# Performance work log

Hardware: AMD Instinct MI355X
Metric: run time of the kernel (lower is better)

The kernel has to match this reference:

```python
import jax, jax.numpy as jnp
import numpy as np

D = 2048
NH = 16
DH = D // NH          # 128
DC = D // 4           # 512  (KV latent)
DCQ = D // 2          # 1024 (Q latent)
B = 1
L = 2048
MAX_LEN = 4096


def precompute_rope(dh, max_len):
    inv_freq = 1.0 / (10000.0 ** (jnp.arange(0, dh, 2, dtype=jnp.float32) / dh))
    t = jnp.arange(max_len, dtype=jnp.float32)
    freqs = jnp.outer(t, inv_freq)                 # [max_len, dh/2]
    emb = jnp.concatenate([freqs, freqs], axis=-1) # [max_len, dh]
    return jnp.cos(emb), jnp.sin(emb)


def apply_rope(t, cos, sin):
    # t: [B, H, L, dh]; cos/sin: [L, dh]
    x1, x2 = jnp.split(t, 2, axis=-1)
    rot = jnp.concatenate([-x2, x1], axis=-1)
    return t * cos + rot * sin


def setup_inputs() -> dict:
    key = jax.random.key(0)
    ks = jax.random.split(key, 9)
    s = 0.02
    return {
        "x": jax.random.normal(ks[0], (B, L, D), dtype=jnp.float32),
        "W_DKV": jax.random.normal(ks[1], (D, DC), dtype=jnp.float32) * s,
        "W_UK": jax.random.normal(ks[2], (DC, NH * DH), dtype=jnp.float32) * s,
        "W_UV": jax.random.normal(ks[3], (DC, NH * DH), dtype=jnp.float32) * s,
        "W_DQ": jax.random.normal(ks[4], (D, DCQ), dtype=jnp.float32) * s,
        "W_UQ": jax.random.normal(ks[5], (DCQ, 2 * NH * DH), dtype=jnp.float32) * s,
        "W_lam": jax.random.normal(ks[6], (D, NH), dtype=jnp.float32) * s,
        "b_lam": jnp.zeros((NH,), dtype=jnp.float32),
        "W_out": jax.random.normal(ks[7], (D, D), dtype=jnp.float32) * s,
    }


def reference(x, W_DKV, W_UK, W_UV, W_DQ, W_UQ, W_lam, b_lam, W_out):
    Bx, Lx, Dx = x.shape
    cos, sin = precompute_rope(DH, MAX_LEN)
    cos, sin = cos[:Lx], sin[:Lx]

    # MLA KV compression: single K/V shared by the paired query heads
    c_kv = x @ W_DKV                                            # [B, L, dc]
    k = (c_kv @ W_UK).reshape(Bx, Lx, NH, DH).transpose(0, 2, 1, 3)   # [B, nh, L, dh]
    v = (c_kv @ W_UV).reshape(Bx, Lx, NH, DH).transpose(0, 2, 1, 3)   # [B, nh, L, dh]

    # Low-rank Q, doubled heads for differential attention
    c_q = x @ W_DQ                                              # [B, L, dcq]
    q = (c_q @ W_UQ).reshape(Bx, Lx, 2 * NH, DH).transpose(0, 2, 1, 3)  # [B, 2nh, L, dh]

    q = apply_rope(q, cos, sin)
    k = apply_rope(k, cos, sin)

    # Group paired heads (2i, 2i+1) share k/v head i -> avoid repeat_interleave
    qp = q.reshape(Bx, NH, 2, Lx, DH)                           # [B, nh, 2, L, dh]
    scale = 1.0 / jnp.sqrt(jnp.asarray(DH, dtype=x.dtype))
    scores = jnp.einsum('bhpqd,bhkd->bhpqk', qp, k) * scale     # [B, nh, 2, L, L]
    causal = jnp.tril(jnp.ones((Lx, Lx), dtype=bool))
    scores = jnp.where(causal, scores, jnp.asarray(-jnp.inf, dtype=scores.dtype))
    probs = jax.nn.softmax(scores, axis=-1)
    attn = jnp.einsum('bhpqk,bhkd->bhpqd', probs, v)            # [B, nh, 2, L, dh]
    attn1, attn2 = attn[:, :, 0], attn[:, :, 1]                 # [B, nh, L, dh]

    # Token-specific sigmoid lambda per head
    lam = jax.nn.sigmoid(x @ W_lam + b_lam)                     # [B, L, nh]
    lam = lam.transpose(0, 2, 1)[..., None]                     # [B, nh, L, 1]

    out = (attn1 - lam * attn2).transpose(0, 2, 1, 3).reshape(Bx, Lx, Dx)
    return out @ W_out
```

## Files before the change

kernel.cpp:

```cpp
#include <hip/hip_runtime.h>
#include <cstdint>
#include <cstddef>

typedef __bf16 bf16x8 __attribute__((ext_vector_type(8)));
typedef __bf16 bf16x4 __attribute__((ext_vector_type(4)));
typedef float f32x4 __attribute__((ext_vector_type(4)));


template <int N> __device__ __forceinline__ void waitcnt_vm() {
  if constexpr (N == 3)      asm volatile("s_waitcnt vmcnt(3)" ::: "memory");
  else if constexpr (N == 4) asm volatile("s_waitcnt vmcnt(4)" ::: "memory");
  else if constexpr (N == 6) asm volatile("s_waitcnt vmcnt(6)" ::: "memory");
  else if constexpr (N == 8) asm volatile("s_waitcnt vmcnt(8)" ::: "memory");
  else                       asm volatile("s_waitcnt vmcnt(0)" ::: "memory");
}

template <int BM, int NKS>
__device__ __forceinline__ void gemm_core(const __bf16* __restrict__ A,
                                          const __bf16* __restrict__ Bt,
                                          int K, int bm, int bn,
                                          __bf16* As, __bf16* Bs,
                                          f32x4 (*acc)[4]) {
  const int tid = threadIdx.x;
  const int w = tid >> 6;
  const int lane = tid & 63;
  const int quad = lane >> 4;
  const int l16 = lane & 15;
  constexpr int WM = (BM == 128) ? 64 : 32;
  constexpr int MI = WM / 16;
  constexpr int NL = NKS * (BM / 64 + 2);
  const int wm = (w & 1) * WM;
  const int wn = (w >> 1) * 64;
  const int srow = lane >> 2;
  const int sseg = (lane & 3) * 8;

  auto stage = [&](int k0, int buf) {
#pragma unroll
    for (int ks = 0; ks < NKS; ++ks) {
#pragma unroll
      for (int g = 0; g < BM / 64; ++g) {
        const int grp = w + g * 4;
        const __bf16* ga = A + (size_t)(bm + grp * 16 + srow) * K + k0 + ks * 32 + sseg;
        __builtin_amdgcn_global_load_lds(
            (const __attribute__((address_space(1))) void*)ga,
            (__attribute__((address_space(3))) void*)&As[(buf * NKS + ks) * (BM * 32) + grp * 512],
            16, 0, 0);
      }
#pragma unroll
      for (int g = 0; g < 2; ++g) {
        const int grp = w + g * 4;
        const __bf16* gb = Bt + (size_t)(bn + grp * 16 + srow) * K + k0 + ks * 32 + sseg;
        __builtin_amdgcn_global_load_lds(
            (const __attribute__((address_space(1))) void*)gb,
            (__attribute__((address_space(3))) void*)&Bs[(buf * NKS + ks) * 4096 + grp * 512],
            16, 0, 0);
      }
    }
  };

#pragma unroll
  for (int i = 0; i < MI; ++i)
#pragma unroll
    for (int j = 0; j < 4; ++j) acc[i][j] = (f32x4){0.f, 0.f, 0.f, 0.f};

  asm volatile("s_waitcnt vmcnt(0)" ::: "memory");
  stage(0, 0);

  const int NIT = K / (32 * NKS);
  for (int it = 0; it < NIT; ++it) {
    const int cur = it & 1;
    if (it + 1 < NIT) {
      stage((it + 1) * 32 * NKS, cur ^ 1);
      waitcnt_vm<NL>();
    } else {
      waitcnt_vm<0>();
    }
    __builtin_amdgcn_s_barrier();
    asm volatile("" ::: "memory");
    const __bf16* Ab = &As[cur * NKS * (BM * 32)];
    const __bf16* Bb = &Bs[cur * NKS * 4096];
#pragma unroll
    for (int ks = 0; ks < NKS; ++ks) {
      bf16x8 af[MI], bfr[4];
#pragma unroll
      for (int i = 0; i < MI; ++i)
        af[i] = *(const bf16x8*)&Ab[ks * (BM * 32) + (wm + i * 16 + l16) * 32 + quad * 8];
#pragma unroll
      for (int j = 0; j < 4; ++j)
        bfr[j] = *(const bf16x8*)&Bb[ks * 4096 + (wn + j * 16 + l16) * 32 + quad * 8];
#pragma unroll
      for (int i = 0; i < MI; ++i)
#pragma unroll
        for (int j = 0; j < 4; ++j)
          acc[i][j] = __builtin_amdgcn_mfma_f32_16x16x32_bf16(af[i], bfr[j],
                                                              acc[i][j], 0, 0, 0);
    }
    asm volatile("s_waitcnt lgkmcnt(0)" ::: "memory");
    __builtin_amdgcn_s_barrier();
    asm volatile("" ::: "memory");
  }
}

template <int BM, int NKS, bool BF16OUT>
__device__ __forceinline__ void gemm_body(const __bf16* __restrict__ A,
                                          const __bf16* __restrict__ Bt,
                                          void* __restrict__ Cv,
                                          int N, int K, int bm, int bn,
                                          __bf16* As, __bf16* Bs) {
  constexpr int MI = (BM == 128) ? 4 : 2;
  constexpr int WM = (BM == 128) ? 64 : 32;
  f32x4 acc[MI][4];
  gemm_core<BM, NKS>(A, Bt, K, bm, bn, As, Bs, acc);
  const int tid = threadIdx.x;
  const int w = tid >> 6, lane = tid & 63, quad = lane >> 4, l16 = lane & 15;
  const int wm = (w & 1) * WM, wn = (w >> 1) * 64;
#pragma unroll
  for (int i = 0; i < MI; ++i)
#pragma unroll
    for (int j = 0; j < 4; ++j)
#pragma unroll
      for (int r = 0; r < 4; ++r) {
        const int row = bm + wm + i * 16 + quad * 4 + r;
        const int col = bn + wn + j * 16 + l16;
        if constexpr (BF16OUT)
          ((__bf16*)Cv)[(size_t)row * N + col] = (__bf16)acc[i][j][r];
        else
          ((float*)Cv)[(size_t)row * N + col] = acc[i][j][r];
      }
}

template <int BM, int NKS, bool BF16OUT>
__global__ __launch_bounds__(256) void gemm_mfma(const __bf16* __restrict__ A,
                                                 const __bf16* __restrict__ Bt,
                                                 void* __restrict__ Cv,
                                                 int M, int N, int K) {
  __shared__ __bf16 As[2 * BM * 32 * NKS];
  __shared__ __bf16 Bs[2 * 128 * 32 * NKS];
  gemm_body<BM, NKS, BF16OUT>(A, Bt, Cv, N, K, blockIdx.y * BM, blockIdx.x * 128, As, Bs);
}

__global__ __launch_bounds__(256) void down_lam(
    const __bf16* __restrict__ x_bf, const __bf16* __restrict__ WtDKV,
    const __bf16* __restrict__ WtDQ, __bf16* __restrict__ c_kv,
    __bf16* __restrict__ c_q, const __bf16* __restrict__ WlT,
    const float* __restrict__ b_lam, float* __restrict__ lam) {
  __shared__ __bf16 As[2 * 64 * 32 * 2];
  __shared__ __bf16 Bs[2 * 128 * 32 * 2];
  const int bx = blockIdx.x;
  const int tid = threadIdx.x;
  if (bx == 12) {
    const int w = tid >> 6, lane = tid & 63, quad = lane >> 4, l16 = lane & 15;
    const int m0 = (blockIdx.y * 4 + w) * 16;
    const __bf16* xrow = x_bf + (size_t)(m0 + l16) * 2048 + quad * 8;
    const __bf16* wrow = WlT + (size_t)l16 * 2048 + quad * 8;
    f32x4 acc[4];
#pragma unroll
    for (int u = 0; u < 4; ++u) acc[u] = (f32x4){0.f, 0.f, 0.f, 0.f};
    for (int k0 = 0; k0 < 2048; k0 += 128) {
#pragma unroll
      for (int u = 0; u < 4; ++u) {
        bf16x8 a = *(const bf16x8*)&xrow[k0 + u * 32];
        bf16x8 b = *(const bf16x8*)&wrow[k0 + u * 32];
        acc[u] = __builtin_amdgcn_mfma_f32_16x16x32_bf16(a, b, acc[u], 0, 0, 0);
      }
    }
    const float bl = b_lam[l16];
#pragma unroll
    for (int r = 0; r < 4; ++r) {
      const float v = acc[0][r] + acc[1][r] + acc[2][r] + acc[3][r] + bl;
      lam[(size_t)(m0 + quad * 4 + r) * 16 + l16] = 1.0f / (1.0f + __expf(-v));
    }
    return;
  }
  if (bx < 4)
    gemm_body<64, 2, true>(x_bf, WtDKV, (void*)c_kv, 512, 2048,
                           blockIdx.y * 64, bx * 128, As, Bs);
  else
    gemm_body<64, 2, true>(x_bf, WtDQ, (void*)c_q, 1024, 2048,
                           blockIdx.y * 64, (bx - 4) * 128, As, Bs);
}

__global__ __launch_bounds__(256) void up_fused3(
    const __bf16* __restrict__ c_kv, const __bf16* __restrict__ WtUK,
    const __bf16* __restrict__ WtUV, const __bf16* __restrict__ c_q,
    const __bf16* __restrict__ WtUQ, __bf16* __restrict__ k_bf,
    __bf16* __restrict__ v_t, __bf16* __restrict__ q_bf,
    const float* __restrict__ cosT, const float* __restrict__ sinT) {
  __shared__ __align__(16) char usm[32768];
  __bf16* As = (__bf16*)usm;
  __bf16* Bs = (__bf16*)(usm + 16384);
  const int bx = blockIdx.x;
  const int bm = blockIdx.y * 128;
  const int tid = threadIdx.x;
  const int w = tid >> 6, lane = tid & 63, quad = lane >> 4, l16 = lane & 15;
  const int wm = (w & 1) * 64, wn = (w >> 1) * 64;
  f32x4 acc[4][4];
  if (bx < 16) {
    const int bn = bx * 128;
    gemm_core<128, 1>(c_kv, WtUK, 512, bm, bn, As, Bs, acc);
    __bf16 (*Kt)[128] = (__bf16(*)[128])usm;
#pragma unroll
    for (int i = 0; i < 4; ++i)
#pragma unroll
      for (int j = 0; j < 4; ++j)
#pragma unroll
        for (int r = 0; r < 4; ++r)
          Kt[wm + i * 16 + quad * 4 + r][wn + j * 16 + l16] = (__bf16)acc[i][j][r];
    __syncthreads();
#pragma unroll
    for (int j = 0; j < 4; ++j) {
      const int d = wn + j * 16 + l16;
      const float sgn = (d < 64) ? -1.f : 1.f;
#pragma unroll
      for (int i = 0; i < 4; ++i)
#pragma unroll
        for (int r = 0; r < 4; ++r) {
          const int lr = wm + i * 16 + quad * 4 + r;
          const int l = bm + lr;
          const float v = (float)Kt[lr][d];
          const float pr = (float)Kt[lr][d ^ 64];
          const float ov = v * cosT[l * 128 + d] + sgn * pr * sinT[l * 128 + d];
          k_bf[(size_t)l * 2048 + bn + d] = (__bf16)ov;
        }
    }
  } else if (bx < 32) {
    const int bn = (bx - 16) * 128;
    gemm_core<128, 1>(c_kv, WtUV, 512, bm, bn, As, Bs, acc);
#pragma unroll
    for (int i = 0; i < 4; ++i)
#pragma unroll
      for (int j = 0; j < 4; ++j) {
        const int d = bn + wn + j * 16 + l16;
        const int l = bm + wm + i * 16 + quad * 4;
        bf16x4 pk = {(__bf16)acc[i][j][0], (__bf16)acc[i][j][1],
                     (__bf16)acc[i][j][2], (__bf16)acc[i][j][3]};
        *(bf16x4*)&v_t[(size_t)d * 2048 + l] = pk;
      }
  } else {
    const int bn = (bx - 32) * 128;
    gemm_core<128, 1>(c_q, WtUQ, 1024, bm, bn, As, Bs, acc);
#pragma unroll
    for (int i = 0; i < 4; ++i)
#pragma unroll
      for (int j = 0; j < 4; ++j)
#pragma unroll
        for (int r = 0; r < 4; ++r) {
          const int row = bm + wm + i * 16 + quad * 4 + r;
          const int col = bn + wn + j * 16 + l16;
          q_bf[(size_t)row * 4096 + col] = (__bf16)acc[i][j][r];
        }
  }
}

__global__ __launch_bounds__(256) void prep_all(
    const float* __restrict__ W_DKV, const float* __restrict__ W_DQ,
    const float* __restrict__ W_UK,  const float* __restrict__ W_UV,
    const float* __restrict__ W_UQ,  const float* __restrict__ W_out,
    const float* __restrict__ x,     const float* __restrict__ W_lam,
    __bf16* __restrict__ tDKV, __bf16* __restrict__ tDQ,
    __bf16* __restrict__ tUK,  __bf16* __restrict__ tUV,
    __bf16* __restrict__ tUQ,  __bf16* __restrict__ tOut,
    __bf16* __restrict__ x_bf, __bf16* __restrict__ WlT,
    float* __restrict__ cosT, float* __restrict__ sinT) {
  __shared__ float T[32][36];
  int t = blockIdx.x;
  const int tid = threadIdx.x;
  if (t < 13312) {
    const float* src; __bf16* dst; int K, N, kx, ny;
    if (t < 1024)      {            src = W_DKV; dst = tDKV; K = 2048; N = 512;  kx = t & 63; ny = t >> 6; }
    else if (t < 3072) { t -= 1024; src = W_DQ;  dst = tDQ;  K = 2048; N = 1024; kx = t & 63; ny = t >> 6; }
    else if (t < 4096) { t -= 3072; src = W_UK;  dst = tUK;  K = 512;  N = 2048; kx = t & 15; ny = t >> 4; }
    else if (t < 5120) { t -= 4096; src = W_UV;  dst = tUV;  K = 512;  N = 2048; kx = t & 15; ny = t >> 4; }
    else if (t < 9216) { t -= 5120; src = W_UQ;  dst = tUQ;  K = 1024; N = 4096; kx = t & 31; ny = t >> 5; }
    else               { t -= 9216; src = W_out; dst = tOut; K = 2048; N = 2048; kx = t & 63; ny = t >> 6; }
    const int k0 = kx * 32;
    const int n0 = ny * 32;
    const int r = tid >> 3;
    const int c = (tid & 7) * 4;
    *(float4*)&T[r][c] = *(const float4*)&src[(size_t)(k0 + r) * N + n0 + c];
    __syncthreads();
    bf16x4 o = {(__bf16)T[c + 0][r], (__bf16)T[c + 1][r],
                (__bf16)T[c + 2][r], (__bf16)T[c + 3][r]};
    *(bf16x4*)&dst[(size_t)(n0 + r) * K + k0 + c] = o;
    return;
  }
  t -= 13312;
  if (t < 4096) {
    const int i = t * 256 + tid;
    float4 v = *(const float4*)&x[(size_t)i * 4];
    bf16x4 o = {(__bf16)v.x, (__bf16)v.y, (__bf16)v.z, (__bf16)v.w};
    *(bf16x4*)&x_bf[(size_t)i * 4] = o;
    return;
  }
  t -= 4096;
  if (t < 1024) {
    const int l = t * 2 + (tid >> 7);
    const int d = tid & 127;
    const int j = d & 63;
    const float inv = exp2f(-(float)j * 0.2076205059304601f);
    const float ang = (float)l * inv;
    cosT[l * 128 + d] = cosf(ang);
    sinT[l * 128 + d] = sinf(ang);
    return;
  }
  t -= 1024;
  {
    const int i = t * 256 + tid;
    const int k = i >> 4, n = i & 15;
    WlT[(size_t)n * 2048 + k] = (__bf16)W_lam[i];
  }
}

__global__ __launch_bounds__(512, 2) void attn_kernel3(
    const __bf16* __restrict__ Qb, const __bf16* __restrict__ Kb,
    const __bf16* __restrict__ Vt, const float* __restrict__ cosT,
    const float* __restrict__ sinT, const float* __restrict__ lam,
    __bf16* __restrict__ y) {
  __shared__ __align__(16) char smem[81920];
  float (*Ex)[132] = (float(*)[132])smem;

  const int bx = blockIdx.x;
  const int qt = 31 - (bx >> 4);
  const int hk = bx & 15;
  const int q0 = qt * 64;
  const int tid = threadIdx.x;
  const int w = tid >> 6, lane = tid & 63, quad = lane >> 4, l16 = lane & 15;
  const int wrow = (w & 3) * 16;
  const int qoff = (2 * hk + (w >> 2)) * 128;
  const int kvoff = hk * 128;
  const float qscale = 0.08838834764831845f;
  char* Pw = smem + 65536 + w * 2048;

  bf16x8 aq[4];
  {
    const int l = q0 + wrow + l16;
    const size_t qbase = (size_t)l * 4096 + qoff + quad * 8;
    bf16x8 raw[4];
#pragma unroll
    for (int ks = 0; ks < 4; ++ks)
      raw[ks] = *(const bf16x8*)&Qb[qbase + ks * 32];
#pragma unroll
    for (int ks = 0; ks < 4; ++ks) {
      const float* cp = &cosT[l * 128 + ks * 32 + quad * 8];
      const float* sp = &sinT[l * 128 + ks * 32 + quad * 8];
#pragma unroll
      for (int j = 0; j < 8; ++j) {
        const float cv = cp[j];
        const float sv = sp[j];
        const float rot = (ks < 2) ? -(float)raw[ks + 2][j] : (float)raw[ks - 2][j];
        aq[ks][j] = (__bf16)(((float)raw[ks][j] * cv + rot * sv) * qscale);
      }
    }
  }

  auto stage = [&](int kt_, char* buf) {
    const int k0_ = kt_ * 64;
    __bf16* Ksb = (__bf16*)buf;
    __bf16* Vsb = (__bf16*)(buf + 16384);
#pragma unroll
    for (int d = 0; d < 2; ++d) {
      const int r0 = w * 8 + d * 4;
      const int row = r0 + (lane >> 4);
      const int ck = (lane & 15) ^ (row & 15);
      const __bf16* ga = Kb + (size_t)(k0_ + row) * 2048 + kvoff + ck * 8;
      __builtin_amdgcn_global_load_lds(
          (const __attribute__((address_space(1))) void*)ga,
          (__attribute__((address_space(3))) void*)&Ksb[r0 * 128], 16, 0, 0);
      const int r0v = w * 16 + d * 8;
      const int rowv = r0v + (lane >> 3);
      const int cv = (lane & 7) ^ (rowv & 7);
      const __bf16* gv = Vt + (size_t)(kvoff + rowv) * 2048 + k0_ + cv * 8;
      __builtin_amdgcn_global_load_lds(
          (const __attribute__((address_space(1))) void*)gv,
          (__attribute__((address_space(3))) void*)&Vsb[r0v * 64], 16, 0, 0);
    }
  };

  f32x4 o[8];
#pragma unroll
  for (int i = 0; i < 8; ++i) o[i] = (f32x4){0.f, 0.f, 0.f, 0.f};
  float m = -1e30f, lsum = 0.f;

  asm volatile("s_waitcnt vmcnt(0)" ::: "memory");
  stage(0, smem);

  for (int kt = 0; kt <= qt; ++kt) {
    const int cur = kt & 1;
    __bf16* Ks = (__bf16*)(smem + cur * 32768);
    __bf16* Vs = (__bf16*)(smem + cur * 32768 + 16384);
    const int k0 = kt * 64;
    if (kt < qt) {
      stage(kt + 1, smem + (cur ^ 1) * 32768);
      asm volatile("s_waitcnt vmcnt(4)" ::: "memory");
    } else {
      asm volatile("s_waitcnt vmcnt(0)" ::: "memory");
    }
    __builtin_amdgcn_s_barrier();
    asm volatile("" ::: "memory");
    f32x4 st[4];
#pragma unroll
    for (int t = 0; t < 4; ++t) st[t] = (f32x4){0.f, 0.f, 0.f, 0.f};
    __builtin_amdgcn_s_setprio(1);
#pragma unroll
    for (int ks = 0; ks < 4; ++ks) {
#pragma unroll
      for (int t = 0; t < 4; ++t) {
        bf16x8 ak = *(bf16x8*)&Ks[(t * 16 + l16) * 128 + (((ks * 4 + quad) ^ l16) << 3)];
        st[t] = __builtin_amdgcn_mfma_f32_16x16x32_bf16(ak, aq[ks], st[t], 0, 0, 0);
      }
    }
    __builtin_amdgcn_s_setprio(0);
    {
      const int q = q0 + wrow + l16;
      float rm = -1e30f;
      if (kt != qt) {
#pragma unroll
        for (int t = 0; t < 4; ++t)
#pragma unroll
          for (int r = 0; r < 4; ++r) rm = fmaxf(rm, st[t][r]);
      } else {
#pragma unroll
        for (int t = 0; t < 4; ++t)
#pragma unroll
          for (int r = 0; r < 4; ++r) {
            const int key = k0 + t * 16 + quad * 4 + r;
            if (key > q) st[t][r] = -1e30f;
            rm = fmaxf(rm, st[t][r]);
          }
      }
      rm = fmaxf(rm, __shfl_xor(rm, 16, 64));
      rm = fmaxf(rm, __shfl_xor(rm, 32, 64));
      const float mn = fmaxf(m, rm);
      float rs = 0.f;
#pragma unroll
      for (int t = 0; t < 4; ++t)
#pragma unroll
        for (int r = 0; r < 4; ++r) {
          st[t][r] = __expf(st[t][r] - mn);
          rs += st[t][r];
        }
      rs += __shfl_xor(rs, 16, 64);
      rs += __shfl_xor(rs, 32, 64);
      if (__any(rm > m)) {
        const float alpha = __expf(m - mn);
        lsum = lsum * alpha + rs;
        m = mn;
#pragma unroll
        for (int r = 0; r < 4; ++r) {
          const float ar = __shfl(alpha, quad * 4 + r, 64);
#pragma unroll
          for (int nt = 0; nt < 8; ++nt) o[nt][r] *= ar;
        }
      } else {
        lsum += rs;
      }
      const int prow = l16;
#pragma unroll
      for (int t = 0; t < 4; ++t) {
        bf16x4 pk = {(__bf16)st[t][0], (__bf16)st[t][1],
                     (__bf16)st[t][2], (__bf16)st[t][3]};
        const int wch = (t * 2 + (quad >> 1)) ^ (prow & 7);
        *(bf16x4*)(Pw + prow * 128 + wch * 16 + (quad & 1) * 8) = pk;
      }
    }
    __builtin_amdgcn_s_setprio(1);
#pragma unroll
    for (int ks = 0; ks < 2; ++ks) {
      const int rch = ((ks * 4 + quad) ^ (l16 & 7)) << 4;
      bf16x8 pa = *(bf16x8*)(Pw + l16 * 128 + rch);
#pragma unroll
      for (int nt = 0; nt < 8; ++nt) {
        bf16x8 bv = *(bf16x8*)&Vs[(nt * 16 + l16) * 64 + (((ks * 4 + quad) ^ (l16 & 7)) << 3)];
        o[nt] = __builtin_amdgcn_mfma_f32_16x16x32_bf16(pa, bv, o[nt], 0, 0, 0);
      }
    }
    __builtin_amdgcn_s_setprio(0);
    asm volatile("s_waitcnt lgkmcnt(0)" ::: "memory");
    __builtin_amdgcn_s_barrier();
    asm volatile("" ::: "memory");
  }
  const float linv = 1.0f / lsum;
  if (w >= 4) {
#pragma unroll
    for (int r = 0; r < 4; ++r) {
      const float inv = __shfl(linv, quad * 4 + r, 64);
      const int rr = wrow + quad * 4 + r;
#pragma unroll
      for (int nt = 0; nt < 8; ++nt)
        Ex[rr][nt * 16 + l16] = o[nt][r] * inv;
    }
  }
  __syncthreads();
  if (w < 4) {
#pragma unroll
    for (int r = 0; r < 4; ++r) {
      const float inv = __shfl(linv, quad * 4 + r, 64);
      const int rr = wrow + quad * 4 + r;
      const int l = q0 + rr;
      const float lm = lam[l * 16 + hk];
      __bf16* dst = y + (size_t)l * 2048 + hk * 128;
#pragma unroll
      for (int nt = 0; nt < 8; ++nt) {
        const float v1 = o[nt][r] * inv;
        dst[nt * 16 + l16] = (__bf16)(v1 - lm * Ex[rr][nt * 16 + l16]);
      }
    }
  }
}

extern "C" void kernel_launch(void* const* d_in, const int* in_sizes, int n_in,
                              void* d_out, int out_size, void* d_ws, size_t ws_size,
                              hipStream_t stream) {
  const float* x     = (const float*)d_in[0];
  const float* W_DKV = (const float*)d_in[1];
  const float* W_UK  = (const float*)d_in[2];
  const float* W_UV  = (const float*)d_in[3];
  const float* W_DQ  = (const float*)d_in[4];
  const float* W_UQ  = (const float*)d_in[5];
  const float* W_lam = (const float*)d_in[6];
  const float* b_lam = (const float*)d_in[7];
  const float* W_out = (const float*)d_in[8];
  float* out = (float*)d_out;

  char* ws = (char*)d_ws;
  #define MB(n) ((size_t)(n) << 20)
  __bf16* x_bf   = (__bf16*)(ws + MB(0));
  __bf16* Wt_DKV = (__bf16*)(ws + MB(8));
  __bf16* Wt_DQ  = (__bf16*)(ws + MB(10));
  __bf16* c_kv   = (__bf16*)(ws + MB(14));
  __bf16* c_q    = (__bf16*)(ws + MB(16));
  __bf16* Wt_UK  = (__bf16*)(ws + MB(20));
  __bf16* Wt_UV  = (__bf16*)(ws + MB(22));
  __bf16* Wt_UQ  = (__bf16*)(ws + MB(24));
  __bf16* k_bf   = (__bf16*)(ws + MB(32));
  __bf16* y_bf   = (__bf16*)(ws + MB(40));
  __bf16* q_bf   = (__bf16*)(ws + MB(48));
  __bf16* v_t    = (__bf16*)(ws + MB(64));
  float*  lam    = (float*)(ws + MB(88));
  float*  cosT   = (float*)(ws + MB(89));
  float*  sinT   = (float*)(ws + MB(90));
  __bf16* WlT    = (__bf16*)(ws + MB(91));
  __bf16* Wt_out = (__bf16*)(ws + MB(92));

  prep_all<<<18560, 256, 0, stream>>>(W_DKV, W_DQ, W_UK, W_UV, W_UQ, W_out,
                                      x, W_lam,
                                      Wt_DKV, Wt_DQ, Wt_UK, Wt_UV, Wt_UQ, Wt_out,
                                      x_bf, WlT, cosT, sinT);
  down_lam<<<dim3(13, 32), 256, 0, stream>>>(x_bf, Wt_DKV, Wt_DQ, c_kv, c_q,
                                             WlT, b_lam, lam);
  up_fused3<<<dim3(64, 16), 256, 0, stream>>>(c_kv, Wt_UK, Wt_UV, c_q, Wt_UQ,
                                              k_bf, v_t, q_bf, cosT, sinT);
  attn_kernel3<<<512, 512, 0, stream>>>(q_bf, k_bf, v_t, cosT, sinT, lam, y_bf);
  gemm_mfma<64, 2, false><<<dim3(16, 32), 256, 0, stream>>>(y_bf, Wt_out, out, 2048, 2048, 2048);
}
```

Measured before the change: 310.6 us.

## Move W_out transpose into attention kernel tail blocks and reorder query tiles

The bf16 transpose of W_out leaves the prep kernel and runs as 2048 extra blocks appended to the attention launch. These blocks can fill compute units that sit idle while the causal attention tiles finish unevenly. The attention blocks are also reordered so the first half of the grid runs query tiles heaviest-first and the second half lightest-first. The cost is a larger grid with a branch at the top of the attention kernel, and the transpose blocks each reserve the full 80 KB of shared memory, which limits how many of them run at once.

Result: faster. 300.5 us (-3.2%).

```diff
diff --git a/kernel.cpp b/kernel.cpp
--- a/kernel.cpp
+++ b/kernel.cpp
@@ -255,24 +255,23 @@
 __global__ __launch_bounds__(256) void prep_all(
     const float* __restrict__ W_DKV, const float* __restrict__ W_DQ,
     const float* __restrict__ W_UK,  const float* __restrict__ W_UV,
-    const float* __restrict__ W_UQ,  const float* __restrict__ W_out,
+    const float* __restrict__ W_UQ,
     const float* __restrict__ x,     const float* __restrict__ W_lam,
     __bf16* __restrict__ tDKV, __bf16* __restrict__ tDQ,
     __bf16* __restrict__ tUK,  __bf16* __restrict__ tUV,
-    __bf16* __restrict__ tUQ,  __bf16* __restrict__ tOut,
+    __bf16* __restrict__ tUQ,
     __bf16* __restrict__ x_bf, __bf16* __restrict__ WlT,
     float* __restrict__ cosT, float* __restrict__ sinT) {
   __shared__ float T[32][36];
   int t = blockIdx.x;
   const int tid = threadIdx.x;
-  if (t < 13312) {
+  if (t < 9216) {
     const float* src; __bf16* dst; int K, N, kx, ny;
     if (t < 1024)      {            src = W_DKV; dst = tDKV; K = 2048; N = 512;  kx = t & 63; ny = t >> 6; }
     else if (t < 3072) { t -= 1024; src = W_DQ;  dst = tDQ;  K = 2048; N = 1024; kx = t & 63; ny = t >> 6; }
     else if (t < 4096) { t -= 3072; src = W_UK;  dst = tUK;  K = 512;  N = 2048; kx = t & 15; ny = t >> 4; }
     else if (t < 5120) { t -= 4096; src = W_UV;  dst = tUV;  K = 512;  N = 2048; kx = t & 15; ny = t >> 4; }
-    else if (t < 9216) { t -= 5120; src = W_UQ;  dst = tUQ;  K = 1024; N = 4096; kx = t & 31; ny = t >> 5; }
-    else               { t -= 9216; src = W_out; dst = tOut; K = 2048; N = 2048; kx = t & 63; ny = t >> 6; }
+    else               { t -= 5120; src = W_UQ;  dst = tUQ;  K = 1024; N = 4096; kx = t & 31; ny = t >> 5; }
     const int k0 = kx * 32;
     const int n0 = ny * 32;
     const int r = tid >> 3;
@@ -284,7 +283,7 @@
     *(bf16x4*)&dst[(size_t)(n0 + r) * K + k0 + c] = o;
     return;
   }
-  t -= 13312;
+  t -= 9216;
   if (t < 4096) {
     const int i = t * 256 + tid;
     float4 v = *(const float4*)&x[(size_t)i * 4];
@@ -315,15 +314,33 @@
     const __bf16* __restrict__ Qb, const __bf16* __restrict__ Kb,
     const __bf16* __restrict__ Vt, const float* __restrict__ cosT,
     const float* __restrict__ sinT, const float* __restrict__ lam,
-    __bf16* __restrict__ y) {
+    __bf16* __restrict__ y, const float* __restrict__ W_out,
+    __bf16* __restrict__ Wt_out) {
   __shared__ __align__(16) char smem[81920];
   float (*Ex)[132] = (float(*)[132])smem;
 
   const int bx = blockIdx.x;
-  const int qt = 31 - (bx >> 4);
-  const int hk = bx & 15;
+  const int tid = threadIdx.x;
+  if (bx >= 512) {
+    const int t = (bx - 512) * 2 + (tid >> 8);
+    const int st = tid & 255;
+    float (*T)[36] = (float(*)[36])(smem + (tid >> 8) * 4608);
+    const int k0 = (t & 63) * 32;
+    const int n0 = (t >> 6) * 32;
+    const int r = st >> 3;
+    const int c = (st & 7) * 4;
+    *(float4*)&T[r][c] = *(const float4*)&W_out[(size_t)(k0 + r) * 2048 + n0 + c];
+    __syncthreads();
+    bf16x4 o = {(__bf16)T[c + 0][r], (__bf16)T[c + 1][r],
+                (__bf16)T[c + 2][r], (__bf16)T[c + 3][r]};
+    *(bf16x4*)&Wt_out[(size_t)(n0 + r) * 2048 + k0 + c] = o;
+    return;
+  }
+  const int hv = bx >> 8;
+  const int ii = bx & 255;
+  const int qt = hv ? (ii >> 4) : 31 - (ii >> 4);
+  const int hk = ii & 15;
   const int q0 = qt * 64;
-  const int tid = threadIdx.x;
   const int w = tid >> 6, lane = tid & 63, quad = lane >> 4, l16 = lane & 15;
   const int wrow = (w & 3) * 16;
   const int qoff = (2 * hk + (w >> 2)) * 128;
@@ -542,14 +559,15 @@
   __bf16* WlT    = (__bf16*)(ws + MB(91));
   __bf16* Wt_out = (__bf16*)(ws + MB(92));
 
-  prep_all<<<18560, 256, 0, stream>>>(W_DKV, W_DQ, W_UK, W_UV, W_UQ, W_out,
+  prep_all<<<14464, 256, 0, stream>>>(W_DKV, W_DQ, W_UK, W_UV, W_UQ,
                                       x, W_lam,
-                                      Wt_DKV, Wt_DQ, Wt_UK, Wt_UV, Wt_UQ, Wt_out,
+                                      Wt_DKV, Wt_DQ, Wt_UK, Wt_UV, Wt_UQ,
                                       x_bf, WlT, cosT, sinT);
   down_lam<<<dim3(13, 32), 256, 0, stream>>>(x_bf, Wt_DKV, Wt_DQ, c_kv, c_q,
                                              WlT, b_lam, lam);
   up_fused3<<<dim3(64, 16), 256, 0, stream>>>(c_kv, Wt_UK, Wt_UV, c_q, Wt_UQ,
                                               k_bf, v_t, q_bf, cosT, sinT);
-  attn_kernel3<<<512, 512, 0, stream>>>(q_bf, k_bf, v_t, cosT, sinT, lam, y_bf);
+  attn_kernel3<<<2560, 512, 0, stream>>>(q_bf, k_bf, v_t, cosT, sinT, lam,
+                                         y_bf, W_out, Wt_out);
   gemm_mfma<64, 2, false><<<dim3(16, 32), 256, 0, stream>>>(y_bf, Wt_out, out, 2048, 2048, 2048);
 }
```
